# Kernel optimization log

Measured on AMD Instinct MI355X. Metric: run time of the kernel, lower is better.

Reference implementation:

```python
import jax, jax.numpy as jnp
import numpy as np

B, S, M = 2, 2048, 2048
NQ, NKV, H = 16, 4, 128
EPS = 1e-6
MAX_WAVELENGTH = 10000.0
NEG_INF = -1e9


def rmsnorm(x, scale, eps=EPS):
    # RMSNorm over head_dim (last axis), computed in fp32.
    xf = x.astype(jnp.float32)
    var = jnp.mean(xf * xf, axis=-1, keepdims=True)
    return (xf * jax.lax.rsqrt(var + eps) * scale).astype(x.dtype)


def rope(x, max_wavelength=MAX_WAVELENGTH, scaling_factor=1.0, start_index=0):
    # x: [b, s, n, h]; keras_hub split-half rotary embedding.
    h = x.shape[-1]
    inv_freq = 1.0 / (max_wavelength ** (jnp.arange(0, h, 2, dtype=jnp.float32) / h))
    pos = (jnp.arange(x.shape[1], dtype=jnp.float32) + start_index) / scaling_factor
    freq = pos[:, None] * inv_freq[None, :]             # [s, h/2]
    emb = jnp.concatenate([freq, freq], axis=-1)        # [s, h]
    cos = jnp.cos(emb)[None, :, None, :]
    sin = jnp.sin(emb)[None, :, None, :]
    x1, x2 = x[..., : h // 2], x[..., h // 2 :]
    rot = jnp.concatenate([-x2, x1], axis=-1)
    return (x * cos + rot * sin).astype(x.dtype)


def setup_inputs() -> dict:
    key = jax.random.key(0)
    ks = jax.random.split(key, 6)
    hidden_states = jax.random.normal(ks[0], (B, S, M), dtype=jnp.float32)
    # causal mask [b, q, k]
    causal = jnp.tril(jnp.ones((S, S), dtype=bool))
    attention_mask = jnp.broadcast_to(causal[None], (B, S, S))
    sq = 0.02
    Wq = jax.random.normal(ks[1], (M, NQ, H), dtype=jnp.float32) * sq
    Wk = jax.random.normal(ks[2], (M, NKV, H), dtype=jnp.float32) * sq
    Wv = jax.random.normal(ks[3], (M, NKV, H), dtype=jnp.float32) * sq
    Wo = jax.random.normal(ks[4], (NQ, H, M), dtype=jnp.float32) * sq
    q_scale = jnp.ones((H,), dtype=jnp.float32)
    k_scale = jnp.ones((H,), dtype=jnp.float32)
    return {
        "hidden_states": hidden_states,
        "attention_mask": attention_mask,
        "Wq": Wq,
        "Wk": Wk,
        "Wv": Wv,
        "Wo": Wo,
        "q_scale": q_scale,
        "k_scale": k_scale,
    }


def reference(hidden_states, attention_mask, Wq, Wk, Wv, Wo, q_scale, k_scale):
    inv_norm = 1.0 / np.sqrt(H)
    groups = NQ // NKV

    q = jnp.einsum("bqm,muh->bquh", hidden_states, Wq)   # [b,q,NQ,H]
    q = rope(rmsnorm(q, q_scale))
    k = jnp.einsum("bkm,mvh->bkvh", hidden_states, Wk)   # [b,k,NKV,H]
    k = rope(rmsnorm(k, k_scale))
    v = jnp.einsum("bkm,mvh->bkvh", hidden_states, Wv)

    # GQA broadcast: repeat each kv head `groups` times consecutively.
    k = jnp.repeat(k, groups, axis=2)
    v = jnp.repeat(v, groups, axis=2)

    scores = jnp.einsum("bquh,bkuh->buqk", q, k) * inv_norm  # [b,u,q,k]
    scores = scores.astype(jnp.float32)
    scores = jnp.where(attention_mask[:, None, :, :], scores, NEG_INF)
    probs = jax.nn.softmax(scores, axis=-1).astype(hidden_states.dtype)

    attn = jnp.einsum("buqk,bkuh->bquh", probs, v)
    out = jnp.einsum("bquh,uhm->bqm", attn, Wo)
    return out
```

## Files before the change

### kernel.cpp

```cpp
#include <hip/hip_runtime.h>
#include <stdint.h>

#define BB 2
#define SS 2048
#define MM 2048
#define NQ 16
#define NKV 4
#define HH 128
#define KVB 64

typedef __attribute__((ext_vector_type(4))) float f32x4;
typedef __attribute__((ext_vector_type(16))) float f32x16;
typedef _Float16 f16x8 __attribute__((ext_vector_type(8)));
typedef _Float16 f16x4 __attribute__((ext_vector_type(4)));
typedef _Float16 f16x2 __attribute__((ext_vector_type(2)));
typedef unsigned int uint4v __attribute__((ext_vector_type(4)));

__device__ __forceinline__ void gll16(const _Float16* g, _Float16* l) {
  __builtin_amdgcn_global_load_lds(
      (__attribute__((address_space(1))) void*)g,
      (__attribute__((address_space(3))) void*)l, 16, 0, 0);
}

__device__ __forceinline__ float fexp2(float x) {
#if __has_builtin(__builtin_amdgcn_exp2f)
  return __builtin_amdgcn_exp2f(x);
#else
  float r;
  asm("v_exp_f32 %0, %1" : "=v"(r) : "v"(x));
  return r;
#endif
}

__device__ __forceinline__ unsigned int pkrtz(float a, float b) {
  return __builtin_bit_cast(unsigned int, __builtin_amdgcn_cvt_pkrtz(a, b));
}

__global__ __launch_bounds__(256) void k_f32_to_f16(const float* __restrict__ in,
                                                    _Float16* __restrict__ out, int n4) {
  int i = blockIdx.x * 256 + threadIdx.x;
  if (i >= n4) return;
  float4 v = ((const float4*)in)[i];
  f16x4 o = { (_Float16)v.x, (_Float16)v.y, (_Float16)v.z, (_Float16)v.w };
  ((f16x4*)out)[i] = o;
}

__global__ __launch_bounds__(256) void k_wtrans(
    const float* __restrict__ Wq, const float* __restrict__ Wk,
    const float* __restrict__ Wv, const float* __restrict__ Wo,
    _Float16* __restrict__ Wqkvt, _Float16* __restrict__ Wot) {
  const int z = blockIdx.z;
  if ((z == 1 || z == 2) && blockIdx.y >= 16) return;
  const float* in = (z == 0) ? Wq : (z == 1) ? Wk : (z == 2) ? Wv : Wo;
  _Float16* out = (z == 3) ? Wot : Wqkvt;
  const int N_in = (z == 1 || z == 2) ? 512 : 2048;
  const int n_off = (z == 1) ? 2048 : (z == 2) ? 2560 : 0;

  __shared__ float tile[32][33];
  const int k0 = blockIdx.x * 32;
  const int n0 = blockIdx.y * 32;
  const int tx = threadIdx.x & 31;
  const int ty = threadIdx.x >> 5;
  #pragma unroll
  for (int r = ty; r < 32; r += 8)
    tile[r][tx] = in[(size_t)(k0 + r) * N_in + n0 + tx];
  __syncthreads();
  #pragma unroll
  for (int r = ty; r < 32; r += 8)
    out[(size_t)(n0 + r + n_off) * 2048 + k0 + tx] = (_Float16)tile[tx][r];
}

__global__ __launch_bounds__(256) void k_vtrans(const _Float16* __restrict__ qkv,
                                                _Float16* __restrict__ VtG) {
  __shared__ _Float16 tile[32][33];
  const int s0 = blockIdx.x * 32;
  const int z = blockIdx.y;
  const int h0 = (z & 3) * 32;
  const int bv = z >> 2;
  const int b = bv >> 2;
  const int hv = bv & 3;
  const int tx = threadIdx.x & 31;
  const int ty = threadIdx.x >> 5;
  #pragma unroll
  for (int r = ty; r < 32; r += 8)
    tile[r][tx] = qkv[(size_t)(b * SS + s0 + r) * 3072 + 2560 + hv * 128 + h0 + tx];
  __syncthreads();
  #pragma unroll
  for (int r = ty; r < 32; r += 8)
    VtG[((size_t)bv * HH + h0 + r) * SS + s0 + tx] = tile[tx][r];
}

template <int FN, bool F16OUT>
__global__ __launch_bounds__(512, 2) void k_gemm256(
    const _Float16* __restrict__ A, const _Float16* __restrict__ Bt,
    void* __restrict__ Cout, int NT_M, int N, int K) {
  __shared__ _Float16 As[2][256 * 64];
  __shared__ _Float16 Bs[2][FN * 64 * 64];

  const int tid = threadIdx.x;
  const int w = tid >> 6;
  const int l = tid & 63;
  const int lr = l & 15;
  const int al4 = l >> 4;
  const int wr = w >> 2;
  const int wc = w & 3;
  const int swz = (lr & 7) << 4;

  const int nwg = gridDim.x;
  const int bid = blockIdx.x;
  const int sbid = (bid & 7) * (nwg >> 3) + (bid >> 3);
  const int bm = (sbid % NT_M) * 256;
  const int bn = (sbid / NT_M) * (FN * 64);
  const int KT = K >> 6;

  const int srow = tid >> 3;
  const int sch = (tid & 7) ^ (srow & 7);
  const _Float16* aSrc = A + (size_t)(bm + srow) * K + sch * 8;
  const _Float16* bSrc = Bt + (size_t)(bn + srow) * K + sch * 8;

  auto stA = [&](int buf, int r, int kt) {
    gll16(aSrc + (size_t)(r * 64) * K + kt * 64, &As[buf][r * 4096 + w * 512]);
  };
  auto stB = [&](int buf, int r, int kt) {
    gll16(bSrc + (size_t)(r * 64) * K + kt * 64, &Bs[buf][r * 4096 + w * 512]);
  };

  f32x4 acc[8][FN] = {};

  stA(0, 0, 0); stA(0, 1, 0); stA(0, 2, 0); stA(0, 3, 0);
  stB(0, 0, 0); stB(0, 1, 0);
  if (FN == 3) stB(0, 2, 0);
  if (KT > 1) {
    stA(1, 0, 1); stA(1, 2, 1); stB(1, 0, 1); stB(1, 1, 1);
    asm volatile("s_waitcnt vmcnt(4)" ::: "memory");
  } else {
    asm volatile("s_waitcnt vmcnt(0)" ::: "memory");
  }
  __builtin_amdgcn_s_barrier();

  for (int t = 0; t < KT; ++t) {
    const int cb = t & 1;
    const char* Ab = (const char*)&As[cb][0];
    const char* Bb = (const char*)&Bs[cb][0];
    f16x8 bF[FN][2];
    #pragma unroll
    for (int ph = 0; ph < 2; ++ph) {
      f16x8 aF[4][2];
      #pragma unroll
      for (int fm = 0; fm < 4; ++fm)
        #pragma unroll
        for (int ks = 0; ks < 2; ++ks) {
          const int row = wr * 128 + (ph * 4 + fm) * 16 + lr;
          aF[fm][ks] = *(const f16x8*)(Ab + row * 128 + (((ks * 4 + al4) * 16) ^ swz));
        }
      if (ph == 0) {
        #pragma unroll
        for (int fn = 0; fn < FN; ++fn)
          #pragma unroll
          for (int ks = 0; ks < 2; ++ks) {
            const int col = wc * (FN * 16) + fn * 16 + lr;
            bF[fn][ks] = *(const f16x8*)(Bb + col * 128 + (((ks * 4 + al4) * 16) ^ swz));
          }
      }
      if (ph == 0 && t + 1 < KT) {
        if (FN == 3) stB(cb ^ 1, 2, t + 1);
        stA(cb ^ 1, 1, t + 1); stA(cb ^ 1, 3, t + 1);
      }
      if (ph == 1 && t + 2 < KT) {
        stA(cb, 0, t + 2); stA(cb, 2, t + 2);
        stB(cb, 0, t + 2); stB(cb, 1, t + 2);
      }
      __builtin_amdgcn_s_barrier();
      asm volatile("s_waitcnt lgkmcnt(0)" ::: "memory");
      __builtin_amdgcn_sched_barrier(0);
      __builtin_amdgcn_s_setprio(1);
      #pragma unroll
      for (int fm = 0; fm < 4; ++fm)
        #pragma unroll
        for (int fn = 0; fn < FN; ++fn)
          #pragma unroll
          for (int ks = 0; ks < 2; ++ks)
            acc[ph * 4 + fm][fn] = __builtin_amdgcn_mfma_f32_16x16x32_f16(
                aF[fm][ks], bF[fn][ks], acc[ph * 4 + fm][fn], 0, 0, 0);
      __builtin_amdgcn_s_setprio(0);
      __builtin_amdgcn_sched_barrier(0);
      if (ph == 0) {
        __builtin_amdgcn_s_barrier();
      } else {
        if (t + 2 < KT) asm volatile("s_waitcnt vmcnt(4)" ::: "memory");
        else            asm volatile("s_waitcnt vmcnt(0)" ::: "memory");
        __builtin_amdgcn_s_barrier();
      }
    }
  }

  #pragma unroll
  for (int fm = 0; fm < 8; ++fm) {
    #pragma unroll
    for (int i = 0; i < 4; ++i) {
      const int row = bm + wr * 128 + fm * 16 + al4 * 4 + i;
      #pragma unroll
      for (int fn = 0; fn < FN; ++fn) {
        const int col = bn + wc * (FN * 16) + fn * 16 + lr;
        if (F16OUT)
          ((_Float16*)Cout)[(size_t)row * N + col] = (_Float16)acc[fm][fn][i];
        else
          ((float*)Cout)[(size_t)row * N + col] = acc[fm][fn][i];
      }
    }
  }
}

__global__ __launch_bounds__(256) void k_normrope(
    const _Float16* __restrict__ qkv,
    const float* __restrict__ q_scale, const float* __restrict__ k_scale,
    _Float16* __restrict__ Qr, _Float16* __restrict__ Kr) {
  const int row = blockIdx.x;
  const int b = row >> 11;
  const int s = row & 2047;
  const int hh = blockIdx.y * 4 + (threadIdx.x >> 6);
  const int l = threadIdx.x & 63;
  const _Float16* src = qkv + (size_t)row * 3072 + hh * 128 + l * 2;
  float x0 = (float)src[0];
  float x1 = (float)src[1];
  float ssum = x0 * x0 + x1 * x1;
  #pragma unroll
  for (int d = 1; d < 64; d <<= 1) ssum += __shfl_xor(ssum, d);
  const float rstd = rsqrtf(ssum * (1.f / 128.f) + 1e-6f);
  const float* scl = (hh < 16) ? q_scale : k_scale;
  x0 *= rstd * scl[2 * l];
  x1 *= rstd * scl[2 * l + 1];
  const float y0 = __shfl_xor(x0, 32);
  const float y1 = __shfl_xor(x1, 32);
  const int j0 = (2 * l) & 63;
  const float kLog = 0.20762050593046014f;
  const float f0 = (float)s * exp2f(-(float)j0 * kLog);
  const float f1 = (float)s * exp2f(-(float)(j0 + 1) * kLog);
  const float c0 = cosf(f0), s0 = sinf(f0);
  const float c1 = cosf(f1), s1 = sinf(f1);
  float r0, r1;
  if (l < 32) { r0 = x0 * c0 - y0 * s0; r1 = x1 * c1 - y1 * s1; }
  else        { r0 = x0 * c0 + y0 * s0; r1 = x1 * c1 + y1 * s1; }
  if (hh < 16) {
    _Float16* dst = Qr + ((size_t)(b * NQ + hh) * SS + s) * HH + 2 * l;
    dst[0] = (_Float16)r0; dst[1] = (_Float16)r1;
  } else {
    _Float16* dst = Kr + ((size_t)(b * NKV + (hh - 16)) * SS + s) * HH + 2 * l;
    dst[0] = (_Float16)r0; dst[1] = (_Float16)r1;
  }
}

__device__ const unsigned char g_tasks[24] = {
  61, 63, 28,
  57, 59, 53, 55, 24,
  49, 51, 45, 47, 20,
  41, 43, 37, 39, 16,
  33, 35, 12,
  8, 4, 0
};

__global__ __launch_bounds__(256, 2) void k_attn(
    const _Float16* __restrict__ Qr, const _Float16* __restrict__ Kr,
    const _Float16* __restrict__ VtG,
    const float* __restrict__ qs, const float* __restrict__ ks,
    float* __restrict__ PartA, float* __restrict__ PartB,
    float* __restrict__ psA, float* __restrict__ psB,
    _Float16* __restrict__ Ao) {
  __shared__ _Float16 Ks[128 * 128];
  __shared__ _Float16 Vs[128 * 128];

  const int tid = threadIdx.x;
  const int w = tid >> 6;
  const int l = tid & 63;
  const int l31 = l & 31;
  const int hi = l >> 5;
  const int sw7 = (l31 & 7) << 4;
  const int bu = blockIdx.x;
  const int b = bu >> 4, u = bu & 15;
  const int kvh = u >> 2;

  const int task = g_tasks[blockIdx.y];
  const int heavy = task & 1;
  const int half = (task >> 1) & 1;
  const int qt = task >> 2;
  const int q0 = qt * 128;
  const int total = 2 * qt + 2;
  const int h0 = ((qt + 2) >> 1) << 1;
  const int t0 = heavy ? (half ? h0 : 0) : 0;
  const int t1 = heavy ? (half ? total : h0) : total;

  float ma = fmaxf(fabsf(qs[l]), fabsf(qs[l + 64]));
  float mb = fmaxf(fabsf(ks[l]), fabsf(ks[l + 64]));
  #pragma unroll
  for (int d = 1; d < 64; d <<= 1) {
    ma = fmaxf(ma, __shfl_xor(ma, d));
    mb = fmaxf(mb, __shfl_xor(mb, d));
  }
  const float M2 = 1.4426950408889634f * ma * mb;
  const float K2 = 0.12752982260735795f;

  const _Float16* Kbase = Kr + (size_t)(b * NKV + kvh) * SS * HH;
  const _Float16* Vbase = VtG + (size_t)(b * NKV + kvh) * HH * SS;

  f16x8 qf[8];
  {
    const _Float16* qp = Qr + ((size_t)(b * NQ + u) * SS + q0 + w * 32 + l31) * HH + hi * 8;
    #pragma unroll
    for (int hs = 0; hs < 8; hs++) {
      qf[hs] = *(const f16x8*)(qp + hs * 16);
      qf[hs] *= (_Float16)K2;
    }
  }

  f32x16 acc0 = {}, acc1 = {}, acc2 = {}, acc3 = {};
  float psum = 0.f;

  auto stage = [&](int m) {
    const int kv0 = m * KVB;
    #pragma unroll
    for (int it = 0; it < 8; it++) {
      const int n = it * 256 + tid;
      const int row = n >> 4, c = n & 15;
      const int cs = c ^ (row & 7);
      gll16(Kbase + (size_t)(kv0 + row) * HH + cs * 8,
            &Ks[(size_t)(it * 256 + w * 64) * 8]);
      gll16(Vbase + (size_t)row * SS + kv0 + cs * 8,
            &Vs[(size_t)(it * 256 + w * 64) * 8]);
    }
  };

  const int qwb = q0 + w * 32;
  const int qlane = qwb + l31;

  for (int m = t0; m < t1; m += 2) {
    stage(m);
    __syncthreads();
    const char* Kb = (const char*)&Ks[0];
    const char* Vb = (const char*)&Vs[0];
    #pragma unroll
    for (int hh2 = 0; hh2 < 2; ++hh2) {
      const int kv0 = m * KVB + hh2 * 64;
      if (kv0 <= qwb + 31) {
        f32x16 S0 = {}, S1 = {};
        __builtin_amdgcn_s_setprio(1);
        #pragma unroll
        for (int hs = 0; hs < 8; hs++) {
          const int ch = hs * 2 + hi;
          f16x8 k0 = *(const f16x8*)(Kb + (hh2 * 64 + l31) * 256 + ((ch << 4) ^ sw7));
          f16x8 k1 = *(const f16x8*)(Kb + (hh2 * 64 + 32 + l31) * 256 + ((ch << 4) ^ sw7));
          S0 = __builtin_amdgcn_mfma_f32_32x32x16_f16(k0, qf[hs], S0, 0, 0, 0);
          S1 = __builtin_amdgcn_mfma_f32_32x32x16_f16(k1, qf[hs], S1, 0, 0, 0);
        }
        __builtin_amdgcn_s_setprio(0);

        const bool domask = (kv0 + 63 > qwb);
        float p0[16], p1[16];
        #pragma unroll
        for (int r = 0; r < 16; r++) {
          const int cr = (r & 3) + 8 * (r >> 2) + 4 * hi;
          float e0 = fexp2(S0[r] - M2);
          float e1 = fexp2(S1[r] - M2);
          if (domask) {
            if (kv0 + cr > qlane) e0 = 0.f;
            if (kv0 + 32 + cr > qlane) e1 = 0.f;
          }
          p0[r] = e0; p1[r] = e1;
          psum += e0 + e1;
        }

        unsigned int pkv[4][4];
        #pragma unroll
        for (int g = 0; g < 4; g++) {
          pkv[0][g] = pkrtz(p0[2 * g], p0[2 * g + 1]);
          pkv[1][g] = pkrtz(p0[8 + 2 * g], p0[9 + 2 * g]);
          pkv[2][g] = pkrtz(p1[2 * g], p1[2 * g + 1]);
          pkv[3][g] = pkrtz(p1[8 + 2 * g], p1[9 + 2 * g]);
        }
        f16x8 pa[4];
        #pragma unroll
        for (int ksx = 0; ksx < 4; ksx++) {
          unsigned int a0 = pkv[ksx][0], a1 = pkv[ksx][1], a2 = pkv[ksx][2], a3 = pkv[ksx][3];
          unsigned int x0 = (unsigned int)__shfl_xor((int)a0, 32);
          unsigned int x1 = (unsigned int)__shfl_xor((int)a1, 32);
          unsigned int x2 = (unsigned int)__shfl_xor((int)a2, 32);
          unsigned int x3 = (unsigned int)__shfl_xor((int)a3, 32);
          uint4v dv;
          dv.x = hi ? x2 : a0;
          dv.y = hi ? x3 : a1;
          dv.z = hi ? a2 : x0;
          dv.w = hi ? a3 : x1;
          pa[ksx] = __builtin_bit_cast(f16x8, dv);
        }

        __builtin_amdgcn_s_setprio(1);
        #pragma unroll
        for (int ksx = 0; ksx < 4; ksx++) {
          const int ch = hh2 * 8 + ksx * 2 + hi;
          f16x8 v0 = *(const f16x8*)(Vb + (0 * 32 + l31) * 256 + ((ch << 4) ^ sw7));
          acc0 = __builtin_amdgcn_mfma_f32_32x32x16_f16(pa[ksx], v0, acc0, 0, 0, 0);
          f16x8 v1 = *(const f16x8*)(Vb + (1 * 32 + l31) * 256 + ((ch << 4) ^ sw7));
          acc1 = __builtin_amdgcn_mfma_f32_32x32x16_f16(pa[ksx], v1, acc1, 0, 0, 0);
          f16x8 v2 = *(const f16x8*)(Vb + (2 * 32 + l31) * 256 + ((ch << 4) ^ sw7));
          acc2 = __builtin_amdgcn_mfma_f32_32x32x16_f16(pa[ksx], v2, acc2, 0, 0, 0);
          f16x8 v3 = *(const f16x8*)(Vb + (3 * 32 + l31) * 256 + ((ch << 4) ^ sw7));
          acc3 = __builtin_amdgcn_mfma_f32_32x32x16_f16(pa[ksx], v3, acc3, 0, 0, 0);
        }
        __builtin_amdgcn_s_setprio(0);
      }
    }
    __syncthreads();
  }

  const float tot = psum + __shfl_xor(psum, 32);
  if (heavy) {
    const int slot = bu * 8 + (qt - 8);
    float* pPart = (half ? PartB : PartA) + (size_t)slot * 16384;
    float* sPart = (half ? psB : psA) + slot * 128;
    if (hi == 0) sPart[w * 32 + l31] = tot;
    #pragma unroll
    for (int r = 0; r < 16; r++) {
      const int cr = (r & 3) + 8 * (r >> 2) + 4 * hi;
      float* dst = pPart + (size_t)(w * 32 + cr) * 128 + l31;
      dst[0]  = acc0[r];
      dst[32] = acc1[r];
      dst[64] = acc2[r];
      dst[96] = acc3[r];
    }
  } else {
    const float inv = 1.f / tot;
    #pragma unroll
    for (int r = 0; r < 16; r++) {
      const int cr = (r & 3) + 8 * (r >> 2) + 4 * hi;
      const float ivr = __shfl(inv, cr);
      _Float16* dst = Ao + ((size_t)(b * SS + q0 + w * 32 + cr)) * MM + u * HH + l31;
      dst[0]  = (_Float16)(acc0[r] * ivr);
      dst[32] = (_Float16)(acc1[r] * ivr);
      dst[64] = (_Float16)(acc2[r] * ivr);
      dst[96] = (_Float16)(acc3[r] * ivr);
    }
  }
}

__global__ __launch_bounds__(256) void k_fin(
    const float* __restrict__ PartA, const float* __restrict__ PartB,
    const float* __restrict__ psA, const float* __restrict__ psB,
    _Float16* __restrict__ Ao) {
  const int slot = blockIdx.x;
  const int bu = slot >> 3, st = slot & 7;
  const int b = bu >> 4, u = bu & 15;
  const int qt = st + 8;
  const float* pa = PartA + (size_t)slot * 16384;
  const float* pb = PartB + (size_t)slot * 16384;
  const float* sa = psA + slot * 128;
  const float* sb = psB + slot * 128;
  #pragma unroll
  for (int it = 0; it < 16; it++) {
    const int unit = it * 256 + threadIdx.x;
    const int qr = unit >> 5, cg = unit & 31;
    const float inv = 1.f / (sa[qr] + sb[qr]);
    f32x4 va = *(const f32x4*)(pa + qr * 128 + cg * 4);
    f32x4 vb = *(const f32x4*)(pb + qr * 128 + cg * 4);
    f16x4 o = { (_Float16)((va[0] + vb[0]) * inv), (_Float16)((va[1] + vb[1]) * inv),
                (_Float16)((va[2] + vb[2]) * inv), (_Float16)((va[3] + vb[3]) * inv) };
    *(f16x4*)(Ao + ((size_t)(b * SS + qt * 128 + qr)) * MM + u * HH + cg * 4) = o;
  }
}

extern "C" void kernel_launch(void* const* d_in, const int* in_sizes, int n_in,
                              void* d_out, int out_size, void* d_ws, size_t ws_size,
                              hipStream_t stream) {
  const float* hidden = (const float*)d_in[0];
  const float* Wq = (const float*)d_in[2];
  const float* Wk = (const float*)d_in[3];
  const float* Wv = (const float*)d_in[4];
  const float* Wo = (const float*)d_in[5];
  const float* q_scale = (const float*)d_in[6];
  const float* k_scale = (const float*)d_in[7];

  char* ws = (char*)d_ws;
  _Float16* Xb    = (_Float16*)(ws);
  _Float16* Wqkvt = (_Float16*)(ws + 16777216);
  _Float16* Wot   = (_Float16*)(ws + 29360128);
  _Float16* qkv   = (_Float16*)(ws + 37748736);
  _Float16* Qr    = (_Float16*)(ws + 62914560);
  _Float16* Kr    = (_Float16*)(ws + 79691776);
  _Float16* VtG   = (_Float16*)(ws + 83886080);
  _Float16* Ao    = (_Float16*)(ws + 88080384);
  float*    PartB = (float*)(ws);
  float*    PartA = (float*)(ws + 37748736);
  float*    psA   = (float*)(ws + 54525952);
  float*    psB   = (float*)(ws + 54657024);

  k_f32_to_f16<<<dim3(8192), dim3(256), 0, stream>>>(hidden, Xb, 2097152);
  k_wtrans<<<dim3(64, 64, 4), dim3(256), 0, stream>>>(Wq, Wk, Wv, Wo, Wqkvt, Wot);
  k_gemm256<3, true><<<dim3(256), dim3(512), 0, stream>>>(Xb, Wqkvt, (void*)qkv, 16, 3072, 2048);
  k_normrope<<<dim3(4096, 5), dim3(256), 0, stream>>>(qkv, q_scale, k_scale, Qr, Kr);
  k_vtrans<<<dim3(64, 32), dim3(256), 0, stream>>>(qkv, VtG);
  k_attn<<<dim3(32, 24), dim3(256), 0, stream>>>(Qr, Kr, VtG, q_scale, k_scale,
                                                 PartA, PartB, psA, psB, Ao);
  k_fin<<<dim3(256), dim3(256), 0, stream>>>(PartA, PartB, psA, psB, Ao);
  k_gemm256<2, false><<<dim3(256), dim3(512), 0, stream>>>(Ao, Wot, d_out, 16, 2048, 2048);
}
```

Before: 210.7 us.

## Merge prep and V-transpose kernels, remap attention blocks to group KV heads

Folds the fp32-to-fp16 activation cast into the weight-transpose kernel and the V transpose into the norm/rope kernel, removing two launches and their inter-kernel gaps. Also reorders the attention grid so that consecutive block IDs cover the four query heads sharing one KV head, with tasks spread across batch and KV groups. The goal is better L2 reuse of K/V tiles and fewer launches. The cost is some idle early-exit blocks in the merged grids, and the normrope kernel now carries a shared tile it does not need on its main path.

```diff
diff --git a/kernel.cpp b/kernel.cpp
--- a/kernel.cpp
+++ b/kernel.cpp
@@ -36,20 +36,21 @@
   return __builtin_bit_cast(unsigned int, __builtin_amdgcn_cvt_pkrtz(a, b));
 }
 
-__global__ __launch_bounds__(256) void k_f32_to_f16(const float* __restrict__ in,
-                                                    _Float16* __restrict__ out, int n4) {
-  int i = blockIdx.x * 256 + threadIdx.x;
-  if (i >= n4) return;
-  float4 v = ((const float4*)in)[i];
-  f16x4 o = { (_Float16)v.x, (_Float16)v.y, (_Float16)v.z, (_Float16)v.w };
-  ((f16x4*)out)[i] = o;
-}
-
-__global__ __launch_bounds__(256) void k_wtrans(
+__global__ __launch_bounds__(256) void k_prep(
+    const float* __restrict__ hidden,
     const float* __restrict__ Wq, const float* __restrict__ Wk,
     const float* __restrict__ Wv, const float* __restrict__ Wo,
+    _Float16* __restrict__ Xb,
     _Float16* __restrict__ Wqkvt, _Float16* __restrict__ Wot) {
   const int z = blockIdx.z;
+  if (z >= 4) {
+    const int bid = (z - 4) * 4096 + blockIdx.y * 64 + blockIdx.x;
+    const int i = bid * 256 + threadIdx.x;
+    float4 v = ((const float4*)hidden)[i];
+    f16x4 o = { (_Float16)v.x, (_Float16)v.y, (_Float16)v.z, (_Float16)v.w };
+    ((f16x4*)Xb)[i] = o;
+    return;
+  }
   if ((z == 1 || z == 2) && blockIdx.y >= 16) return;
   const float* in = (z == 0) ? Wq : (z == 1) ? Wk : (z == 2) ? Wv : Wo;
   _Float16* out = (z == 3) ? Wot : Wqkvt;
@@ -68,26 +69,6 @@
   #pragma unroll
   for (int r = ty; r < 32; r += 8)
     out[(size_t)(n0 + r + n_off) * 2048 + k0 + tx] = (_Float16)tile[tx][r];
-}
-
-__global__ __launch_bounds__(256) void k_vtrans(const _Float16* __restrict__ qkv,
-                                                _Float16* __restrict__ VtG) {
-  __shared__ _Float16 tile[32][33];
-  const int s0 = blockIdx.x * 32;
-  const int z = blockIdx.y;
-  const int h0 = (z & 3) * 32;
-  const int bv = z >> 2;
-  const int b = bv >> 2;
-  const int hv = bv & 3;
-  const int tx = threadIdx.x & 31;
-  const int ty = threadIdx.x >> 5;
-  #pragma unroll
-  for (int r = ty; r < 32; r += 8)
-    tile[r][tx] = qkv[(size_t)(b * SS + s0 + r) * 3072 + 2560 + hv * 128 + h0 + tx];
-  __syncthreads();
-  #pragma unroll
-  for (int r = ty; r < 32; r += 8)
-    VtG[((size_t)bv * HH + h0 + r) * SS + s0 + tx] = tile[tx][r];
 }
 
 template <int FN, bool F16OUT>
@@ -214,7 +195,28 @@
 __global__ __launch_bounds__(256) void k_normrope(
     const _Float16* __restrict__ qkv,
     const float* __restrict__ q_scale, const float* __restrict__ k_scale,
-    _Float16* __restrict__ Qr, _Float16* __restrict__ Kr) {
+    _Float16* __restrict__ Qr, _Float16* __restrict__ Kr,
+    _Float16* __restrict__ VtG) {
+  __shared__ _Float16 vtile[32][33];
+  if (blockIdx.y == 5) {
+    if (blockIdx.x >= 2048) return;
+    const int s0 = (blockIdx.x & 63) * 32;
+    const int zz = blockIdx.x >> 6;
+    const int h0 = (zz & 3) * 32;
+    const int bv = zz >> 2;
+    const int b = bv >> 2;
+    const int hv = bv & 3;
+    const int tx = threadIdx.x & 31;
+    const int ty = threadIdx.x >> 5;
+    #pragma unroll
+    for (int r = ty; r < 32; r += 8)
+      vtile[r][tx] = qkv[(size_t)(b * SS + s0 + r) * 3072 + 2560 + hv * 128 + h0 + tx];
+    __syncthreads();
+    #pragma unroll
+    for (int r = ty; r < 32; r += 8)
+      VtG[((size_t)bv * HH + h0 + r) * SS + s0 + tx] = vtile[tx][r];
+    return;
+  }
   const int row = blockIdx.x;
   const int b = row >> 11;
   const int s = row & 2047;
@@ -275,11 +277,17 @@
   const int l31 = l & 31;
   const int hi = l >> 5;
   const int sw7 = (l31 & 7) << 4;
-  const int bu = blockIdx.x;
-  const int b = bu >> 4, u = bu & 15;
-  const int kvh = u >> 2;
-
-  const int task = g_tasks[blockIdx.y];
+
+  const int n = blockIdx.y * 32 + blockIdx.x;
+  const int g = n & 7;
+  const int slot9 = n >> 3;
+  const int j = slot9 & 3;
+  const int b = g >> 2;
+  const int kvh = g & 3;
+  const int u = kvh * 4 + j;
+  const int bu = b * 16 + u;
+
+  const int task = g_tasks[slot9 >> 2];
   const int heavy = task & 1;
   const int half = (task >> 1) & 1;
   const int qt = task >> 2;
@@ -319,8 +327,8 @@
     const int kv0 = m * KVB;
     #pragma unroll
     for (int it = 0; it < 8; it++) {
-      const int n = it * 256 + tid;
-      const int row = n >> 4, c = n & 15;
+      const int nn = it * 256 + tid;
+      const int row = nn >> 4, c = nn & 15;
       const int cs = c ^ (row & 7);
       gll16(Kbase + (size_t)(kv0 + row) * HH + cs * 8,
             &Ks[(size_t)(it * 256 + w * 64) * 8]);
@@ -370,11 +378,11 @@
 
         unsigned int pkv[4][4];
         #pragma unroll
-        for (int g = 0; g < 4; g++) {
-          pkv[0][g] = pkrtz(p0[2 * g], p0[2 * g + 1]);
-          pkv[1][g] = pkrtz(p0[8 + 2 * g], p0[9 + 2 * g]);
-          pkv[2][g] = pkrtz(p1[2 * g], p1[2 * g + 1]);
-          pkv[3][g] = pkrtz(p1[8 + 2 * g], p1[9 + 2 * g]);
+        for (int gg = 0; gg < 4; gg++) {
+          pkv[0][gg] = pkrtz(p0[2 * gg], p0[2 * gg + 1]);
+          pkv[1][gg] = pkrtz(p0[8 + 2 * gg], p0[9 + 2 * gg]);
+          pkv[2][gg] = pkrtz(p1[2 * gg], p1[2 * gg + 1]);
+          pkv[3][gg] = pkrtz(p1[8 + 2 * gg], p1[9 + 2 * gg]);
         }
         f16x8 pa[4];
         #pragma unroll
@@ -491,11 +499,9 @@
   float*    psA   = (float*)(ws + 54525952);
   float*    psB   = (float*)(ws + 54657024);
 
-  k_f32_to_f16<<<dim3(8192), dim3(256), 0, stream>>>(hidden, Xb, 2097152);
-  k_wtrans<<<dim3(64, 64, 4), dim3(256), 0, stream>>>(Wq, Wk, Wv, Wo, Wqkvt, Wot);
+  k_prep<<<dim3(64, 64, 6), dim3(256), 0, stream>>>(hidden, Wq, Wk, Wv, Wo, Xb, Wqkvt, Wot);
   k_gemm256<3, true><<<dim3(256), dim3(512), 0, stream>>>(Xb, Wqkvt, (void*)qkv, 16, 3072, 2048);
-  k_normrope<<<dim3(4096, 5), dim3(256), 0, stream>>>(qkv, q_scale, k_scale, Qr, Kr);
-  k_vtrans<<<dim3(64, 32), dim3(256), 0, stream>>>(qkv, VtG);
+  k_normrope<<<dim3(4096, 6), dim3(256), 0, stream>>>(qkv, q_scale, k_scale, Qr, Kr, VtG);
   k_attn<<<dim3(32, 24), dim3(256), 0, stream>>>(Qr, Kr, VtG, q_scale, k_scale,
                                                  PartA, PartB, psA, psB, Ao);
   k_fin<<<dim3(256), dim3(256), 0, stream>>>(PartA, PartB, psA, psB, Ao);
```

After: 205.5 us. 2.5% less time.
